# Performance work log

Measured on AMD Instinct MI355X. Metric: run time of the kernel, lower is better.

## Reference

```python
import jax, jax.numpy as jnp
import numpy as np

C = 384
NUM_HEADS = 12
WS = 12  # window side
N = WS * WS  # tokens per window = 144
NW = 144  # windows per image
BATCH = 8

def setup_inputs() -> dict:
    key = jax.random.key(0)
    k1, k2, k3, k4, k5, k6, k7 = jax.random.split(key, 7)
    x = jax.random.normal(k1, (BATCH, NW, WS, WS, C), dtype=jnp.float32)
    mask = jax.random.normal(k2, (NW, N, N), dtype=jnp.float32)
    s = 1.0 / np.sqrt(C)
    qkv_w = jax.random.normal(k3, (3 * C, C), dtype=jnp.float32) * s
    qkv_b = jax.random.normal(k4, (3 * C,), dtype=jnp.float32) * 0.02
    proj_w = jax.random.normal(k5, (C, C), dtype=jnp.float32) * s
    proj_b = jax.random.normal(k6, (C,), dtype=jnp.float32) * 0.02
    return {"x": x, "mask": mask, "qkv_w": qkv_w, "qkv_b": qkv_b,
            "proj_w": proj_w, "proj_b": proj_b}

def reference(x, mask, qkv_w, qkv_b, proj_w, proj_b):
    B, nW = x.shape[0], x.shape[1]
    head_dim = C // NUM_HEADS
    scale = head_dim ** -0.5
    # (B_, N, C) windowed tokens
    xw = x.reshape(B * nW, N, C)
    qkv = jnp.einsum('bnc,dc->bnd', xw, qkv_w) + qkv_b  # (B_, N, 3C)
    qkv = qkv.reshape(B * nW, N, 3, NUM_HEADS, head_dim)
    q = qkv[:, :, 0].transpose(0, 2, 1, 3) * scale  # (B_, H, N, hd)
    k = qkv[:, :, 1].transpose(0, 2, 1, 3)
    v = qkv[:, :, 2].transpose(0, 2, 1, 3)
    attn = jnp.einsum('bhnd,bhmd->bhnm', q, k)  # (B_, H, N, N)
    # add window mask: view as (B, nW, H, N, N) + mask[None, :, None]
    attn = attn.reshape(B, nW, NUM_HEADS, N, N) + mask[None, :, None, :, :]
    attn = jax.nn.softmax(attn.reshape(B * nW, NUM_HEADS, N, N), axis=-1)
    out = jnp.einsum('bhnm,bhmd->bhnd', attn, v)  # (B_, H, N, hd)
    out = out.transpose(0, 2, 1, 3).reshape(B * nW, N, C)
    out = jnp.einsum('bnc,dc->bnd', out, proj_w) + proj_b
    return out
```

## Files before the change

kernel.cpp:

```cpp
#include <hip/hip_runtime.h>
#include <stdint.h>

#define TOK 144
#define CD  384
#define NH  12
#define HDIM 32
#define NWIN 1152
#define MASKW 144
#define NQKV 1152

typedef __bf16 bf16_t;
typedef __bf16 bf16x4 __attribute__((ext_vector_type(4)));
typedef __bf16 bf16x8 __attribute__((ext_vector_type(8)));
typedef float  f32x4  __attribute__((ext_vector_type(4)));

__device__ __forceinline__ void gload16(const void* g, void* l) {
    __builtin_amdgcn_global_load_lds(
        (const __attribute__((address_space(1))) uint32_t*)g,
        (__attribute__((address_space(3))) uint32_t*)l, 16, 0, 0);
}

__global__ __launch_bounds__(256) void kconv(const float* __restrict__ qkvw,
                                             const float* __restrict__ projw,
                                             bf16_t* __restrict__ wq,
                                             bf16_t* __restrict__ wp)
{
    int i = (blockIdx.x * 256 + threadIdx.x) * 4;
    const int NQ = NQKV * CD;
    if (i < NQ) {
        float4 v = *(const float4*)(qkvw + i);
        bf16x4 o = {(bf16_t)v.x, (bf16_t)v.y, (bf16_t)v.z, (bf16_t)v.w};
        *(bf16x4*)(wq + i) = o;
    } else {
        int j = i - NQ;
        if (j < CD * CD) {
            float4 v = *(const float4*)(projw + j);
            bf16x4 o = {(bf16_t)v.x, (bf16_t)v.y, (bf16_t)v.z, (bf16_t)v.w};
            *(bf16x4*)(wp + j) = o;
        }
    }
}

__global__ __launch_bounds__(256) void kmask(const float* __restrict__ mask,
                                             float* __restrict__ maskR)
{
    int t = blockIdx.x * 256 + threadIdx.x;
    int lane = t & 63;
    int g = t >> 6;
    int nt = g % 9;
    int g2 = g / 9;
    int wv = g2 % 9;
    int wm = g2 / 9;
    const float* src = mask + (size_t)wm * 20736
                     + (wv * 16 + (lane >> 4) * 4) * 144 + nt * 16 + (lane & 15);
    f32x4 v = { src[0], src[144], src[288], src[432] };
    *(f32x4*)(maskR + (size_t)t * 4) = v;
}

__global__ __launch_bounds__(256) void kx(const float* __restrict__ x,
                                          bf16_t* __restrict__ xb, int n8)
{
    int i = blockIdx.x * 256 + threadIdx.x;
    if (i < n8) {
        float4 a = *(const float4*)(x + (size_t)i * 8);
        float4 b = *(const float4*)(x + (size_t)i * 8 + 4);
        bf16x8 o = {(bf16_t)a.x, (bf16_t)a.y, (bf16_t)a.z, (bf16_t)a.w,
                    (bf16_t)b.x, (bf16_t)b.y, (bf16_t)b.z, (bf16_t)b.w};
        *(bf16x8*)(xb + (size_t)i * 8) = o;
    }
}

__global__ __launch_bounds__(256) void k_qkv(const bf16_t* __restrict__ xb,
                                             const bf16_t* __restrict__ wB,
                                             const float* __restrict__ bias,
                                             bf16_t* __restrict__ Qp,
                                             bf16_t* __restrict__ Kp,
                                             bf16_t* __restrict__ VTp)
{
    int nwg = gridDim.x;
    int orig = blockIdx.x;
    int q8 = nwg >> 3, r8 = nwg & 7;
    int xcd = orig & 7, idx = orig >> 3;
    int wgid = (xcd < r8 ? xcd * (q8 + 1) : r8 * (q8 + 1) + (xcd - r8) * q8) + idx;
    int mb = wgid / 9, nb = wgid % 9;

    __shared__ union SMem {
        struct { bf16_t A[128 * 64]; bf16_t B[128 * 64]; } st;
        bf16_t tile[128 * 136];
    } sm;
    bf16_t* As = sm.st.A;
    bf16_t* Bs = sm.st.B;

    int tid = threadIdx.x;
    int lane = tid & 63, wid = tid >> 6;
    int wr = (wid >> 1) * 64, wc = (wid & 1) * 64;
    int l15 = lane & 15, l4 = lane >> 4;
    int lr8 = lane >> 3, lc8 = lane & 7;

    f32x4 acc[4][4] = {};

    const size_t arow0 = (size_t)mb * 128;
    const bf16_t* aG = xb + (arow0 + (size_t)(wid * 4) * 8 + lr8) * 384 + lc8 * 8;
    const bf16_t* bG = wB + ((size_t)nb * 128 + (size_t)(wid * 4) * 8 + lr8) * 384 + lc8 * 8;

    for (int kk = 0; kk < 6; ++kk) {
        #pragma unroll
        for (int p = 0; p < 4; ++p)
            gload16(aG + (size_t)p * (8 * 384) + kk * 64, As + (wid * 4 + p) * 512);
        #pragma unroll
        for (int p = 0; p < 4; ++p)
            gload16(bG + (size_t)p * (8 * 384) + kk * 64, Bs + (wid * 4 + p) * 512);
        __syncthreads();

        #pragma unroll
        for (int kh = 0; kh < 2; ++kh) {
            bf16x8 af[4], bfr[4];
            #pragma unroll
            for (int i = 0; i < 4; ++i)
                af[i] = *(const bf16x8*)&As[(wr + i * 16 + l15) * 64 + kh * 32 + l4 * 8];
            #pragma unroll
            for (int j = 0; j < 4; ++j)
                bfr[j] = *(const bf16x8*)&Bs[(wc + j * 16 + l15) * 64 + kh * 32 + l4 * 8];
            #pragma unroll
            for (int i = 0; i < 4; ++i)
                #pragma unroll
                for (int j = 0; j < 4; ++j)
                    acc[i][j] = __builtin_amdgcn_mfma_f32_16x16x32_bf16(af[i], bfr[j], acc[i][j], 0, 0, 0);
        }
        __syncthreads();
    }

    const int S = 136;
    const float SCALE = 0.17677669529663687f;
    float scl = (nb < 3) ? SCALE : 1.0f;
    float bv[4];
    #pragma unroll
    for (int j = 0; j < 4; ++j) bv[j] = bias[nb * 128 + wc + j * 16 + l15];

    #pragma unroll
    for (int i = 0; i < 4; ++i)
        #pragma unroll
        for (int j = 0; j < 4; ++j)
            #pragma unroll
            for (int r = 0; r < 4; ++r)
                sm.tile[(wr + i * 16 + l4 * 4 + r) * S + wc + j * 16 + l15] =
                    (bf16_t)((acc[i][j][r] + bv[j]) * scl);
    __syncthreads();

    if (nb < 6) {
        bf16_t* dst = (nb < 3) ? Qp : Kp;
        int db0 = (nb % 3) * 128;
        #pragma unroll
        for (int it = 0; it < 8; ++it) {
            int item = tid + it * 256;
            int row = item >> 4, ch = item & 15;
            bf16x8 v = *(const bf16x8*)&sm.tile[row * S + ch * 8];
            int gr = mb * 128 + row;
            int lw = gr / 144, n = gr - lw * 144;
            int dl = db0 + ch * 8;
            int h = dl >> 5, c32 = dl & 31;
            *(bf16x8*)(dst + (size_t)(lw * 12 + h) * 4608 + n * 32 + c32) = v;
        }
    } else {
        int db0 = (nb - 6) * 128;
        #pragma unroll
        for (int it = 0; it < 8; ++it) {
            int item = tid + it * 256;
            int dl = item & 127;
            int nc = item >> 7;
            int gr0 = mb * 128 + nc * 8;
            int lw = gr0 / 144, n0 = gr0 - lw * 144;
            int rr = db0 + dl;
            int h = rr >> 5, j32 = rr & 31;
            bf16x8 v;
            #pragma unroll
            for (int q = 0; q < 8; ++q)
                v[q] = sm.tile[(nc * 8 + q) * S + dl];
            *(bf16x8*)(VTp + (size_t)(lw * 12 + h) * 4608 + j32 * 144 + n0) = v;
        }
    }
}

__global__ __launch_bounds__(576) void k_attn(const bf16_t* __restrict__ Qp,
                                              const bf16_t* __restrict__ Kp,
                                              const bf16_t* __restrict__ VTp,
                                              const float* __restrict__ maskR,
                                              bf16_t* __restrict__ ao,
                                              int w0)
{
    extern __shared__ char smem[];
    bf16_t* kb  = (bf16_t*)smem;
    bf16_t* vtb = kb + 144 * 40;
    bf16_t* pb  = vtb + 32 * 168;

    int nwg = gridDim.x;
    int orig = blockIdx.x;
    int q8 = nwg >> 3, r8 = nwg & 7;
    int xcd = orig & 7, idx = orig >> 3;
    int wgid = (xcd < r8 ? xcd * (q8 + 1) : r8 * (q8 + 1) + (xcd - r8) * q8) + idx;

    int bw = wgid / 12, h = wgid % 12;
    int W = w0 + bw;
    int wm = W % MASKW;
    size_t base = (size_t)(bw * 12 + h) * 4608;
    int tid = threadIdx.x;

    {
        int row = tid >> 2, c8 = (tid & 3) * 8;
        *(uint4*)&kb[row * 40 + c8] = *(const uint4*)(Kp + base + row * 32 + c8);
        int j = tid / 18, seg = tid % 18;
        *(uint4*)&vtb[j * 168 + seg * 8] = *(const uint4*)(VTp + base + j * 144 + seg * 8);
        if (tid < 64) {
            int jj = tid >> 1, cc = 144 + (tid & 1) * 8;
            uint4 z = {0, 0, 0, 0};
            *(uint4*)&vtb[jj * 168 + cc] = z;
        }
    }
    __syncthreads();

    int lane = tid & 63, wv = tid >> 6;
    int l15 = lane & 15, l4 = lane >> 4;
    int row16 = wv * 16;

    bf16x8 aq = *(const bf16x8*)(Qp + base + (row16 + l15) * 32 + l4 * 8);

    const float* mR = maskR + ((size_t)(wm * 9 + wv) * 9) * 256 + lane * 4;
    f32x4 s[9];
    #pragma unroll
    for (int nt = 0; nt < 9; ++nt) {
        bf16x8 bk = *(const bf16x8*)&kb[(nt * 16 + l15) * 40 + l4 * 8];
        f32x4 mv = *(const f32x4*)(mR + nt * 256);
        s[nt] = __builtin_amdgcn_mfma_f32_16x16x32_bf16(aq, bk, mv, 0, 0, 0);
    }

    float mx[4], sm[4];
    #pragma unroll
    for (int r = 0; r < 4; ++r) {
        float m = s[0][r];
        #pragma unroll
        for (int nt = 1; nt < 9; ++nt) m = fmaxf(m, s[nt][r]);
        #pragma unroll
        for (int off = 1; off < 16; off <<= 1) m = fmaxf(m, __shfl_xor(m, off, 64));
        mx[r] = m;
    }
    #pragma unroll
    for (int r = 0; r < 4; ++r) {
        float sum = 0.f;
        #pragma unroll
        for (int nt = 0; nt < 9; ++nt) {
            float e = __expf(s[nt][r] - mx[r]);
            s[nt][r] = e;
            sum += e;
        }
        #pragma unroll
        for (int off = 1; off < 16; off <<= 1) sum += __shfl_xor(sum, off, 64);
        sm[r] = sum;
    }

    #pragma unroll
    for (int nt = 0; nt < 9; ++nt)
        #pragma unroll
        for (int r = 0; r < 4; ++r)
            pb[(row16 + l4 * 4 + r) * 168 + nt * 16 + l15] = (bf16_t)s[nt][r];
    {
        int rr = lane >> 2, cc = 144 + (lane & 3) * 4;
        uint2 z = {0, 0};
        *(uint2*)&pb[(row16 + rr) * 168 + cc] = z;
    }
    f32x4 o0 = {0.f, 0.f, 0.f, 0.f}, o1 = {0.f, 0.f, 0.f, 0.f};
    #pragma unroll
    for (int ks = 0; ks < 5; ++ks) {
        bf16x8 ap  = *(const bf16x8*)&pb[(row16 + l15) * 168 + ks * 32 + l4 * 8];
        bf16x8 bv0 = *(const bf16x8*)&vtb[(l15) * 168 + ks * 32 + l4 * 8];
        bf16x8 bv1 = *(const bf16x8*)&vtb[(16 + l15) * 168 + ks * 32 + l4 * 8];
        o0 = __builtin_amdgcn_mfma_f32_16x16x32_bf16(ap, bv0, o0, 0, 0, 0);
        o1 = __builtin_amdgcn_mfma_f32_16x16x32_bf16(ap, bv1, o1, 0, 0, 0);
    }
    float inv[4];
    #pragma unroll
    for (int r = 0; r < 4; ++r) inv[r] = 1.0f / sm[r];
    bf16_t* ob = pb + row16 * 168;
    #pragma unroll
    for (int r = 0; r < 4; ++r) {
        ob[(l4 * 4 + r) * 32 + l15]      = (bf16_t)(o0[r] * inv[r]);
        ob[(l4 * 4 + r) * 32 + 16 + l15] = (bf16_t)(o1[r] * inv[r]);
    }
    bf16x8 v = *(const bf16x8*)&ob[(lane >> 2) * 32 + (lane & 3) * 8];
    *(bf16x8*)(ao + ((size_t)bw * 144 + row16 + (lane >> 2)) * 384 + h * 32 + (lane & 3) * 8) = v;
}

__global__ __launch_bounds__(256) void k_proj(const bf16_t* __restrict__ ao,
                                              const bf16_t* __restrict__ wp,
                                              const float* __restrict__ bias,
                                              float* __restrict__ out,
                                              int rowoff)
{
    int nwg = gridDim.x;
    int orig = blockIdx.x;
    int q8 = nwg >> 3, r8 = nwg & 7;
    int xcd = orig & 7, idx = orig >> 3;
    int wgid = (xcd < r8 ? xcd * (q8 + 1) : r8 * (q8 + 1) + (xcd - r8) * q8) + idx;
    int mb = wgid / 3, nb = wgid % 3;

    __shared__ union SMem {
        struct { bf16_t A[128 * 64]; bf16_t B[128 * 64]; } st;
        float tile[128 * 68];
    } sm;
    bf16_t* As = sm.st.A;
    bf16_t* Bs = sm.st.B;

    int tid = threadIdx.x;
    int lane = tid & 63, wid = tid >> 6;
    int wr = (wid >> 1) * 64, wc = (wid & 1) * 64;
    int l15 = lane & 15, l4 = lane >> 4;
    int lr8 = lane >> 3, lc8 = lane & 7;

    f32x4 acc[4][4] = {};

    const bf16_t* aG = ao + ((size_t)mb * 128 + (size_t)(wid * 4) * 8 + lr8) * 384 + lc8 * 8;
    const bf16_t* bG = wp + ((size_t)nb * 128 + (size_t)(wid * 4) * 8 + lr8) * 384 + lc8 * 8;

    for (int kk = 0; kk < 6; ++kk) {
        #pragma unroll
        for (int p = 0; p < 4; ++p)
            gload16(aG + (size_t)p * (8 * 384) + kk * 64, As + (wid * 4 + p) * 512);
        #pragma unroll
        for (int p = 0; p < 4; ++p)
            gload16(bG + (size_t)p * (8 * 384) + kk * 64, Bs + (wid * 4 + p) * 512);
        __syncthreads();

        #pragma unroll
        for (int kh = 0; kh < 2; ++kh) {
            bf16x8 af[4], bfr[4];
            #pragma unroll
            for (int i = 0; i < 4; ++i)
                af[i] = *(const bf16x8*)&As[(wr + i * 16 + l15) * 64 + kh * 32 + l4 * 8];
            #pragma unroll
            for (int j = 0; j < 4; ++j)
                bfr[j] = *(const bf16x8*)&Bs[(wc + j * 16 + l15) * 64 + kh * 32 + l4 * 8];
            #pragma unroll
            for (int i = 0; i < 4; ++i)
                #pragma unroll
                for (int j = 0; j < 4; ++j)
                    acc[i][j] = __builtin_amdgcn_mfma_f32_16x16x32_bf16(af[i], bfr[j], acc[i][j], 0, 0, 0);
        }
        __syncthreads();
    }

    float bv[4];
    #pragma unroll
    for (int j = 0; j < 4; ++j) bv[j] = bias[nb * 128 + wc + j * 16 + l15];

    #pragma unroll
    for (int half = 0; half < 2; ++half) {
        if (half) __syncthreads();
        if ((wid & 1) == half) {
            #pragma unroll
            for (int i = 0; i < 4; ++i)
                #pragma unroll
                for (int j = 0; j < 4; ++j)
                    #pragma unroll
                    for (int r = 0; r < 4; ++r)
                        sm.tile[(wr + i * 16 + l4 * 4 + r) * 68 + j * 16 + l15] =
                            acc[i][j][r] + bv[j];
        }
        __syncthreads();
        #pragma unroll
        for (int it = 0; it < 8; ++it) {
            int item = tid + it * 256;
            int row = item >> 4, ch = item & 15;
            float4 v = *(const float4*)&sm.tile[row * 68 + ch * 4];
            *(float4*)(out + (size_t)(rowoff + mb * 128 + row) * 384
                           + nb * 128 + half * 64 + ch * 4) = v;
        }
    }
}

extern "C" void kernel_launch(void* const* d_in, const int* in_sizes, int n_in,
                              void* d_out, int out_size, void* d_ws, size_t ws_size,
                              hipStream_t stream)
{
    const float* x     = (const float*)d_in[0];
    const float* mask  = (const float*)d_in[1];
    const float* qkvw  = (const float*)d_in[2];
    const float* qkvb  = (const float*)d_in[3];
    const float* projw = (const float*)d_in[4];
    const float* projb = (const float*)d_in[5];
    float* out = (float*)d_out;

    char* ws = (char*)d_ws;
    bf16_t* WQ   = (bf16_t*)ws;
    bf16_t* WP   = (bf16_t*)(ws + 884736);
    float* maskR = (float*)(ws + 1179648);
    char* chunkbase = ws + 13123584;

    size_t avail = ws_size > 13123584 ? ws_size - 13123584 : 0;
    long cw = (long)(avail / 552960);
    cw = (cw / 16) * 16;
    if (cw > NWIN) cw = NWIN;
    if (cw < 16) cw = 16;

    size_t qbytes = (size_t)cw * 110592;
    bf16_t* Xb  = (bf16_t*)chunkbase;
    bf16_t* Qp  = (bf16_t*)(chunkbase + qbytes);
    bf16_t* Kp  = (bf16_t*)(chunkbase + 2 * qbytes);
    bf16_t* VTp = (bf16_t*)(chunkbase + 3 * qbytes);
    bf16_t* AO  = (bf16_t*)(chunkbase + 4 * qbytes);

    kconv<<<576, 256, 0, stream>>>(qkvw, projw, WQ, WP);
    kmask<<<2916, 256, 0, stream>>>(mask, maskR);

    for (int w0 = 0; w0 < NWIN; w0 += (int)cw) {
        int c = (int)((NWIN - w0) < cw ? (NWIN - w0) : cw);
        int n8 = c * 6912;
        kx<<<(n8 + 255) / 256, 256, 0, stream>>>(x + (size_t)w0 * 144 * 384, Xb, n8);
        int mblocks = (c * 144) / 128;
        k_qkv<<<mblocks * 9, 256, 0, stream>>>(Xb, WQ, qkvb, Qp, Kp, VTp);
        k_attn<<<c * 12, 576, 70656, stream>>>(Qp, Kp, VTp, maskR, AO, w0);
        k_proj<<<mblocks * 3, 256, 0, stream>>>(AO, WP, projb, out, w0 * 144);
    }
}
```

Before: 661.1 us.

## Prepack weights in MFMA fragment order, double-buffer A tiles with swizzled LDS

Weights are pre-packed into MFMA B-fragment order, with the Q scale folded into the weights. The QKV and projection GEMMs then read B fragments straight from global memory instead of staging them through LDS. The A operand (activations) is double-buffered in LDS with an XOR swizzle, so the next k-slice loads while the current one computes, with one barrier per iteration instead of two. Since the weights are already scaled, the epilogue only scales the bias. The risk is higher global-load latency on the B fragments, which are no longer shared through LDS across waves.

```diff
diff --git a/kernel.cpp b/kernel.cpp
--- a/kernel.cpp
+++ b/kernel.cpp
@@ -20,24 +20,44 @@
         (__attribute__((address_space(3))) uint32_t*)l, 16, 0, 0);
 }
 
-__global__ __launch_bounds__(256) void kconv(const float* __restrict__ qkvw,
+__global__ __launch_bounds__(256) void kpack(const float* __restrict__ qkvw,
                                              const float* __restrict__ projw,
-                                             bf16_t* __restrict__ wq,
-                                             bf16_t* __restrict__ wp)
-{
-    int i = (blockIdx.x * 256 + threadIdx.x) * 4;
-    const int NQ = NQKV * CD;
-    if (i < NQ) {
-        float4 v = *(const float4*)(qkvw + i);
-        bf16x4 o = {(bf16_t)v.x, (bf16_t)v.y, (bf16_t)v.z, (bf16_t)v.w};
-        *(bf16x4*)(wq + i) = o;
+                                             bf16_t* __restrict__ WQf,
+                                             bf16_t* __restrict__ WPf)
+{
+    int t = blockIdx.x * 256 + threadIdx.x;
+    const int NQU = 55296;
+    const float SCALE = 0.17677669529663687f;
+    if (t < NQU) {
+        int lane = t & 63;
+        int jj = (t >> 6) & 7;
+        int kh = (t >> 9) & 1;
+        int rest = t >> 10;
+        int kk = rest % 6, nb = rest / 6;
+        int d = nb * 128 + jj * 16 + (lane & 15);
+        int k = kk * 64 + kh * 32 + (lane >> 4) * 8;
+        const float* src = qkvw + (size_t)d * 384 + k;
+        float4 a = *(const float4*)src;
+        float4 b = *(const float4*)(src + 4);
+        float s = (d < 384) ? SCALE : 1.0f;
+        bf16x8 o = {(bf16_t)(a.x*s), (bf16_t)(a.y*s), (bf16_t)(a.z*s), (bf16_t)(a.w*s),
+                    (bf16_t)(b.x*s), (bf16_t)(b.y*s), (bf16_t)(b.z*s), (bf16_t)(b.w*s)};
+        *(bf16x8*)(WQf + (size_t)t * 8) = o;
     } else {
-        int j = i - NQ;
-        if (j < CD * CD) {
-            float4 v = *(const float4*)(projw + j);
-            bf16x4 o = {(bf16_t)v.x, (bf16_t)v.y, (bf16_t)v.z, (bf16_t)v.w};
-            *(bf16x4*)(wp + j) = o;
-        }
+        int u = t - NQU;
+        int lane = u & 63;
+        int jj = (u >> 6) & 7;
+        int kh = (u >> 9) & 1;
+        int rest = u >> 10;
+        int kk = rest % 6, nb = rest / 6;
+        int d = nb * 128 + jj * 16 + (lane & 15);
+        int k = kk * 64 + kh * 32 + (lane >> 4) * 8;
+        const float* src = projw + (size_t)d * 384 + k;
+        float4 a = *(const float4*)src;
+        float4 b = *(const float4*)(src + 4);
+        bf16x8 o = {(bf16_t)a.x, (bf16_t)a.y, (bf16_t)a.z, (bf16_t)a.w,
+                    (bf16_t)b.x, (bf16_t)b.y, (bf16_t)b.z, (bf16_t)b.w};
+        *(bf16x8*)(WPf + (size_t)u * 8) = o;
     }
 }
 
@@ -71,7 +91,7 @@
 }
 
 __global__ __launch_bounds__(256) void k_qkv(const bf16_t* __restrict__ xb,
-                                             const bf16_t* __restrict__ wB,
+                                             const bf16_t* __restrict__ WQf,
                                              const float* __restrict__ bias,
                                              bf16_t* __restrict__ Qp,
                                              bf16_t* __restrict__ Kp,
@@ -85,57 +105,62 @@
     int mb = wgid / 9, nb = wgid % 9;
 
     __shared__ union SMem {
-        struct { bf16_t A[128 * 64]; bf16_t B[128 * 64]; } st;
+        bf16_t A[2][128 * 64];
         bf16_t tile[128 * 136];
     } sm;
-    bf16_t* As = sm.st.A;
-    bf16_t* Bs = sm.st.B;
 
     int tid = threadIdx.x;
     int lane = tid & 63, wid = tid >> 6;
     int wr = (wid >> 1) * 64, wc = (wid & 1) * 64;
     int l15 = lane & 15, l4 = lane >> 4;
     int lr8 = lane >> 3, lc8 = lane & 7;
+    int lc8s = lc8 ^ lr8;
 
     f32x4 acc[4][4] = {};
 
-    const size_t arow0 = (size_t)mb * 128;
-    const bf16_t* aG = xb + (arow0 + (size_t)(wid * 4) * 8 + lr8) * 384 + lc8 * 8;
-    const bf16_t* bG = wB + ((size_t)nb * 128 + (size_t)(wid * 4) * 8 + lr8) * 384 + lc8 * 8;
+    const bf16_t* aG = xb + ((size_t)mb * 128 + wid * 32 + lr8) * 384 + lc8s * 8;
+
+    #pragma unroll
+    for (int p = 0; p < 4; ++p)
+        gload16(aG + (size_t)p * (8 * 384), &sm.A[0][(wid * 4 + p) * 512]);
 
     for (int kk = 0; kk < 6; ++kk) {
-        #pragma unroll
-        for (int p = 0; p < 4; ++p)
-            gload16(aG + (size_t)p * (8 * 384) + kk * 64, As + (wid * 4 + p) * 512);
-        #pragma unroll
-        for (int p = 0; p < 4; ++p)
-            gload16(bG + (size_t)p * (8 * 384) + kk * 64, Bs + (wid * 4 + p) * 512);
+        int buf = kk & 1;
         __syncthreads();
-
+        if (kk < 5) {
+            #pragma unroll
+            for (int p = 0; p < 4; ++p)
+                gload16(aG + (size_t)p * (8 * 384) + (kk + 1) * 64,
+                        &sm.A[buf ^ 1][(wid * 4 + p) * 512]);
+        }
         #pragma unroll
         for (int kh = 0; kh < 2; ++kh) {
             bf16x8 af[4], bfr[4];
             #pragma unroll
-            for (int i = 0; i < 4; ++i)
-                af[i] = *(const bf16x8*)&As[(wr + i * 16 + l15) * 64 + kh * 32 + l4 * 8];
-            #pragma unroll
             for (int j = 0; j < 4; ++j)
-                bfr[j] = *(const bf16x8*)&Bs[(wc + j * 16 + l15) * 64 + kh * 32 + l4 * 8];
+                bfr[j] = *(const bf16x8*)(WQf +
+                    ((((size_t)(nb * 6 + kk) * 2 + kh) * 8 + (wid & 1) * 4 + j) * 64 + lane) * 8);
+            #pragma unroll
+            for (int i = 0; i < 4; ++i) {
+                int row = wr + i * 16 + l15;
+                int slot = (kh * 4 + l4) ^ (l15 & 7);
+                af[i] = *(const bf16x8*)&sm.A[buf][row * 64 + slot * 8];
+            }
             #pragma unroll
             for (int i = 0; i < 4; ++i)
                 #pragma unroll
                 for (int j = 0; j < 4; ++j)
                     acc[i][j] = __builtin_amdgcn_mfma_f32_16x16x32_bf16(af[i], bfr[j], acc[i][j], 0, 0, 0);
         }
-        __syncthreads();
-    }
+    }
+    __syncthreads();
 
     const int S = 136;
     const float SCALE = 0.17677669529663687f;
     float scl = (nb < 3) ? SCALE : 1.0f;
     float bv[4];
     #pragma unroll
-    for (int j = 0; j < 4; ++j) bv[j] = bias[nb * 128 + wc + j * 16 + l15];
+    for (int j = 0; j < 4; ++j) bv[j] = bias[nb * 128 + wc + j * 16 + l15] * scl;
 
     #pragma unroll
     for (int i = 0; i < 4; ++i)
@@ -144,7 +169,7 @@
             #pragma unroll
             for (int r = 0; r < 4; ++r)
                 sm.tile[(wr + i * 16 + l4 * 4 + r) * S + wc + j * 16 + l15] =
-                    (bf16_t)((acc[i][j][r] + bv[j]) * scl);
+                    (bf16_t)(acc[i][j][r] + bv[j]);
     __syncthreads();
 
     if (nb < 6) {
@@ -290,7 +315,7 @@
 }
 
 __global__ __launch_bounds__(256) void k_proj(const bf16_t* __restrict__ ao,
-                                              const bf16_t* __restrict__ wp,
+                                              const bf16_t* __restrict__ WPf,
                                               const float* __restrict__ bias,
                                               float* __restrict__ out,
                                               int rowoff)
@@ -303,49 +328,55 @@
     int mb = wgid / 3, nb = wgid % 3;
 
     __shared__ union SMem {
-        struct { bf16_t A[128 * 64]; bf16_t B[128 * 64]; } st;
+        bf16_t A[2][128 * 64];
         float tile[128 * 68];
     } sm;
-    bf16_t* As = sm.st.A;
-    bf16_t* Bs = sm.st.B;
 
     int tid = threadIdx.x;
     int lane = tid & 63, wid = tid >> 6;
     int wr = (wid >> 1) * 64, wc = (wid & 1) * 64;
     int l15 = lane & 15, l4 = lane >> 4;
     int lr8 = lane >> 3, lc8 = lane & 7;
+    int lc8s = lc8 ^ lr8;
 
     f32x4 acc[4][4] = {};
 
-    const bf16_t* aG = ao + ((size_t)mb * 128 + (size_t)(wid * 4) * 8 + lr8) * 384 + lc8 * 8;
-    const bf16_t* bG = wp + ((size_t)nb * 128 + (size_t)(wid * 4) * 8 + lr8) * 384 + lc8 * 8;
+    const bf16_t* aG = ao + ((size_t)mb * 128 + wid * 32 + lr8) * 384 + lc8s * 8;
+
+    #pragma unroll
+    for (int p = 0; p < 4; ++p)
+        gload16(aG + (size_t)p * (8 * 384), &sm.A[0][(wid * 4 + p) * 512]);
 
     for (int kk = 0; kk < 6; ++kk) {
-        #pragma unroll
-        for (int p = 0; p < 4; ++p)
-            gload16(aG + (size_t)p * (8 * 384) + kk * 64, As + (wid * 4 + p) * 512);
-        #pragma unroll
-        for (int p = 0; p < 4; ++p)
-            gload16(bG + (size_t)p * (8 * 384) + kk * 64, Bs + (wid * 4 + p) * 512);
+        int buf = kk & 1;
         __syncthreads();
-
+        if (kk < 5) {
+            #pragma unroll
+            for (int p = 0; p < 4; ++p)
+                gload16(aG + (size_t)p * (8 * 384) + (kk + 1) * 64,
+                        &sm.A[buf ^ 1][(wid * 4 + p) * 512]);
+        }
         #pragma unroll
         for (int kh = 0; kh < 2; ++kh) {
             bf16x8 af[4], bfr[4];
             #pragma unroll
-            for (int i = 0; i < 4; ++i)
-                af[i] = *(const bf16x8*)&As[(wr + i * 16 + l15) * 64 + kh * 32 + l4 * 8];
-            #pragma unroll
             for (int j = 0; j < 4; ++j)
-                bfr[j] = *(const bf16x8*)&Bs[(wc + j * 16 + l15) * 64 + kh * 32 + l4 * 8];
+                bfr[j] = *(const bf16x8*)(WPf +
+                    ((((size_t)(nb * 6 + kk) * 2 + kh) * 8 + (wid & 1) * 4 + j) * 64 + lane) * 8);
+            #pragma unroll
+            for (int i = 0; i < 4; ++i) {
+                int row = wr + i * 16 + l15;
+                int slot = (kh * 4 + l4) ^ (l15 & 7);
+                af[i] = *(const bf16x8*)&sm.A[buf][row * 64 + slot * 8];
+            }
             #pragma unroll
             for (int i = 0; i < 4; ++i)
                 #pragma unroll
                 for (int j = 0; j < 4; ++j)
                     acc[i][j] = __builtin_amdgcn_mfma_f32_16x16x32_bf16(af[i], bfr[j], acc[i][j], 0, 0, 0);
         }
-        __syncthreads();
-    }
+    }
+    __syncthreads();
 
     float bv[4];
     #pragma unroll
@@ -389,8 +420,8 @@
     float* out = (float*)d_out;
 
     char* ws = (char*)d_ws;
-    bf16_t* WQ   = (bf16_t*)ws;
-    bf16_t* WP   = (bf16_t*)(ws + 884736);
+    bf16_t* WQf  = (bf16_t*)ws;
+    bf16_t* WPf  = (bf16_t*)(ws + 884736);
     float* maskR = (float*)(ws + 1179648);
     char* chunkbase = ws + 13123584;
 
@@ -407,7 +438,7 @@
     bf16_t* VTp = (bf16_t*)(chunkbase + 3 * qbytes);
     bf16_t* AO  = (bf16_t*)(chunkbase + 4 * qbytes);
 
-    kconv<<<576, 256, 0, stream>>>(qkvw, projw, WQ, WP);
+    kpack<<<288, 256, 0, stream>>>(qkvw, projw, WQf, WPf);
     kmask<<<2916, 256, 0, stream>>>(mask, maskR);
 
     for (int w0 = 0; w0 < NWIN; w0 += (int)cw) {
@@ -415,8 +446,8 @@
         int n8 = c * 6912;
         kx<<<(n8 + 255) / 256, 256, 0, stream>>>(x + (size_t)w0 * 144 * 384, Xb, n8);
         int mblocks = (c * 144) / 128;
-        k_qkv<<<mblocks * 9, 256, 0, stream>>>(Xb, WQ, qkvb, Qp, Kp, VTp);
+        k_qkv<<<mblocks * 9, 256, 0, stream>>>(Xb, WQf, qkvb, Qp, Kp, VTp);
         k_attn<<<c * 12, 576, 70656, stream>>>(Qp, Kp, VTp, maskR, AO, w0);
-        k_proj<<<mblocks * 3, 256, 0, stream>>>(AO, WP, projb, out, w0 * 144);
-    }
-}
+        k_proj<<<mblocks * 3, 256, 0, stream>>>(AO, WPf, projb, out, w0 * 144);
+    }
+}
```

Measured after the change: 647.6 us. 1.02x faster.
